# Kernel optimization log

Hardware: AMD Instinct MI355X
Metric: run time of the kernel (lower is better)

Reference implementation:

```python
import jax, jax.numpy as jnp
import numpy as np

D = 8192  # n_out, already a power of two so D_adjusted == D
BATCH = 4096


def fwht(x):
    """Unnormalized fast Walsh-Hadamard transform along axis 0 (H @ x).
    x: (D, M) -> (D, M). Loop is over log2(D) butterfly stages (structural)."""
    Dn = x.shape[0]
    M = x.shape[1]
    h = 1
    while h < Dn:
        x = x.reshape(Dn // (2 * h), 2, h, M)
        a, b = x[:, 0], x[:, 1]
        x = jnp.stack([a + b, a - b], axis=1).reshape(Dn, M)
        h *= 2
    return x


def setup_inputs() -> dict:
    key = jax.random.key(0)
    k_x, k_s1, k_s2, k_rho, k_eps = jax.random.split(key, 5)
    return {
        "x": jax.random.normal(k_x, (BATCH, 1), dtype=jnp.float32),
        "s1": jax.random.normal(k_s1, (D,), dtype=jnp.float32),
        "s2": jax.random.normal(k_s2, (D,), dtype=jnp.float32),
        "g_mu": jnp.zeros((D,), dtype=jnp.float32),
        "g_rho": jax.random.uniform(k_rho, (D,), dtype=jnp.float32) - 3.0,
        "epsilon": jax.random.normal(k_eps, (D,), dtype=jnp.float32),
    }


def reference(x, s1, s2, g_mu, g_rho, epsilon):
    # variational sample g_tilde ~ N(g_mu, softplus(g_rho)^2)
    g_sigma = jax.nn.softplus(g_rho)
    g_tilde = g_mu + g_sigma * epsilon                      # (D,)
    # W = diag(s1) @ H @ diag(g_tilde) @ H @ diag(s2)
    W = s1[:, None] * fwht(g_tilde[:, None] * fwht(jnp.diag(s2)))  # (D, D)
    # column matrix: first D entries of row-major flatten, shape (D, 1)
    w_col = W.reshape(-1)[:D]                               # (D,)
    # F.linear(x, w_col[:, None]) == x @ w_col[None, :]
    return x @ w_col[None, :]                               # (BATCH, D)
```

## Files before the change

kernel.cpp:

```cpp
#include <hip/hip_runtime.h>
#include <math.h>


#define WHVI_D 8192
#define WHVI_BATCH 4096

typedef float v4f __attribute__((ext_vector_type(4)));

__global__ __launch_bounds__(1024) void whvi_fwht_wcol(
    const float* __restrict__ s1, const float* __restrict__ s2,
    const float* __restrict__ g_mu, const float* __restrict__ g_rho,
    const float* __restrict__ eps, float* __restrict__ w) {
  __shared__ float s[WHVI_D];
  const int tid = threadIdx.x;

  {
    const float4* mu4 = (const float4*)g_mu;
    const float4* rh4 = (const float4*)g_rho;
    const float4* ep4 = (const float4*)eps;
    for (int i = tid; i < WHVI_D / 4; i += 1024) {
      float4 m = mu4[i], r = rh4[i], e = ep4[i];
      float4 g;
      g.x = m.x + (fmaxf(r.x, 0.0f) + log1pf(expf(-fabsf(r.x)))) * e.x;
      g.y = m.y + (fmaxf(r.y, 0.0f) + log1pf(expf(-fabsf(r.y)))) * e.y;
      g.z = m.z + (fmaxf(r.z, 0.0f) + log1pf(expf(-fabsf(r.z)))) * e.z;
      g.w = m.w + (fmaxf(r.w, 0.0f) + log1pf(expf(-fabsf(r.w)))) * e.w;
      ((float4*)s)[i] = g;
    }
  }

  for (int h = 1; h < WHVI_D; h <<= 1) {
    __syncthreads();
    for (int p = tid; p < WHVI_D / 2; p += 1024) {
      int k = p & (h - 1);
      int i = ((p - k) << 1) + k;
      float a = s[i];
      float b = s[i + h];
      s[i]     = a + b;
      s[i + h] = a - b;
    }
  }
  __syncthreads();

  const float s10 = s1[0];
  {
    const float4* s24 = (const float4*)s2;
    float4* w4 = (float4*)w;
    for (int i = tid; i < WHVI_D / 4; i += 1024) {
      float4 t = ((float4*)s)[i];
      float4 c = s24[i];
      float4 o;
      o.x = s10 * c.x * t.x;
      o.y = s10 * c.y * t.y;
      o.z = s10 * c.z * t.z;
      o.w = s10 * c.w * t.w;
      w4[i] = o;
    }
  }
}

__global__ __launch_bounds__(256) void whvi_outer(
    const float* __restrict__ x, const float* __restrict__ w,
    float* __restrict__ out) {
  const int b = blockIdx.x;
  const float xb = x[b];
  const v4f* __restrict__ w4 = (const v4f*)w;
  v4f* __restrict__ o4 = (v4f*)(out + (size_t)b * WHVI_D);

  v4f v[8];
  #pragma unroll
  for (int t = 0; t < 8; ++t) v[t] = w4[threadIdx.x + t * 256];
  #pragma unroll
  for (int t = 0; t < 8; ++t) {
    v4f r = xb * v[t];
    __builtin_nontemporal_store(r, &o4[threadIdx.x + t * 256]);
  }
}

extern "C" void kernel_launch(void* const* d_in, const int* in_sizes, int n_in,
                              void* d_out, int out_size, void* d_ws, size_t ws_size,
                              hipStream_t stream) {
  const float* x     = (const float*)d_in[0];
  const float* s1    = (const float*)d_in[1];
  const float* s2    = (const float*)d_in[2];
  const float* g_mu  = (const float*)d_in[3];
  const float* g_rho = (const float*)d_in[4];
  const float* eps   = (const float*)d_in[5];
  float* out = (float*)d_out;
  float* w   = (float*)d_ws;

  whvi_fwht_wcol<<<1, 1024, 0, stream>>>(s1, s2, g_mu, g_rho, eps, w);
  whvi_outer<<<WHVI_BATCH, 256, 0, stream>>>(x, w, out);
}
```

Before: 162.6 us.

## Fuse FWHT and outer product into one kernel with redundant per-block transform

Merges the single-block FWHT kernel and the outer-product kernel into one launch, with each of 512 blocks of 1024 threads recomputing the full 8192-point transform in shared memory and then writing 8 output rows. This removes the serial single-block kernel, the workspace round trip and the second launch. In exchange every block repeats the 13-stage butterfly, adding redundant compute and sync before its stores, and the large blocks with 32KB shared memory may limit occupancy for the store phase.

Result: no change. 162.1 us (-0.3%).

```diff
diff --git a/kernel.cpp b/kernel.cpp
--- a/kernel.cpp
+++ b/kernel.cpp
@@ -4,13 +4,15 @@
 
 #define WHVI_D 8192
 #define WHVI_BATCH 4096
+#define ROWS_PER_BLOCK 8
 
 typedef float v4f __attribute__((ext_vector_type(4)));
 
-__global__ __launch_bounds__(1024) void whvi_fwht_wcol(
-    const float* __restrict__ s1, const float* __restrict__ s2,
-    const float* __restrict__ g_mu, const float* __restrict__ g_rho,
-    const float* __restrict__ eps, float* __restrict__ w) {
+__global__ __launch_bounds__(1024) void whvi_fused(
+    const float* __restrict__ x, const float* __restrict__ s1,
+    const float* __restrict__ s2, const float* __restrict__ g_mu,
+    const float* __restrict__ g_rho, const float* __restrict__ eps,
+    float* __restrict__ out) {
   __shared__ float s[WHVI_D];
   const int tid = threadIdx.x;
 
@@ -18,7 +20,9 @@
     const float4* mu4 = (const float4*)g_mu;
     const float4* rh4 = (const float4*)g_rho;
     const float4* ep4 = (const float4*)eps;
-    for (int i = tid; i < WHVI_D / 4; i += 1024) {
+    #pragma unroll
+    for (int t = 0; t < 2; ++t) {
+      int i = tid + t * 1024;
       float4 m = mu4[i], r = rh4[i], e = ep4[i];
       float4 g;
       g.x = m.x + (fmaxf(r.x, 0.0f) + log1pf(expf(-fabsf(r.x)))) * e.x;
@@ -31,7 +35,9 @@
 
   for (int h = 1; h < WHVI_D; h <<= 1) {
     __syncthreads();
-    for (int p = tid; p < WHVI_D / 2; p += 1024) {
+    #pragma unroll
+    for (int t = 0; t < 4; ++t) {
+      int p = tid + t * 1024;
       int k = p & (h - 1);
       int i = ((p - k) << 1) + k;
       float a = s[i];
@@ -43,37 +49,19 @@
   __syncthreads();
 
   const float s10 = s1[0];
-  {
-    const float4* s24 = (const float4*)s2;
-    float4* w4 = (float4*)w;
-    for (int i = tid; i < WHVI_D / 4; i += 1024) {
-      float4 t = ((float4*)s)[i];
-      float4 c = s24[i];
-      float4 o;
-      o.x = s10 * c.x * t.x;
-      o.y = s10 * c.y * t.y;
-      o.z = s10 * c.z * t.z;
-      o.w = s10 * c.w * t.w;
-      w4[i] = o;
-    }
-  }
-}
+  const v4f* s24 = (const v4f*)s2;
+  const v4f* sh4 = (const v4f*)s;
+  v4f w0 = (s10 * s24[tid]) * sh4[tid];
+  v4f w1 = (s10 * s24[tid + 1024]) * sh4[tid + 1024];
 
-__global__ __launch_bounds__(256) void whvi_outer(
-    const float* __restrict__ x, const float* __restrict__ w,
-    float* __restrict__ out) {
-  const int b = blockIdx.x;
-  const float xb = x[b];
-  const v4f* __restrict__ w4 = (const v4f*)w;
-  v4f* __restrict__ o4 = (v4f*)(out + (size_t)b * WHVI_D);
-
-  v4f v[8];
+  const int row0 = blockIdx.x * ROWS_PER_BLOCK;
   #pragma unroll
-  for (int t = 0; t < 8; ++t) v[t] = w4[threadIdx.x + t * 256];
-  #pragma unroll
-  for (int t = 0; t < 8; ++t) {
-    v4f r = xb * v[t];
-    __builtin_nontemporal_store(r, &o4[threadIdx.x + t * 256]);
+  for (int r = 0; r < ROWS_PER_BLOCK; ++r) {
+    const int row = row0 + r;
+    const float xb = x[row];
+    v4f* o4 = (v4f*)(out + (size_t)row * WHVI_D);
+    __builtin_nontemporal_store(xb * w0, &o4[tid]);
+    __builtin_nontemporal_store(xb * w1, &o4[tid + 1024]);
   }
 }
 
@@ -87,8 +75,7 @@
   const float* g_rho = (const float*)d_in[4];
   const float* eps   = (const float*)d_in[5];
   float* out = (float*)d_out;
-  float* w   = (float*)d_ws;
 
-  whvi_fwht_wcol<<<1, 1024, 0, stream>>>(s1, s2, g_mu, g_rho, eps, w);
-  whvi_outer<<<WHVI_BATCH, 256, 0, stream>>>(x, w, out);
+  whvi_fused<<<WHVI_BATCH / ROWS_PER_BLOCK, 1024, 0, stream>>>(
+      x, s1, s2, g_mu, g_rho, eps, out);
 }
```
